# Optimization experiments

Hardware: AMD Instinct MI355X
Metric: run time of the kernel (lower is better)

The kernel has to match this reference:

```python
import jax, jax.numpy as jnp
import numpy as np

BEAM = 5  # config['beam_size']

def layer_norm(x, g, b, eps=1e-5):
    mu = jnp.mean(x, -1, keepdims=True)
    var = jnp.var(x, -1, keepdims=True)
    return (x - mu) / jnp.sqrt(var + eps) * g + b

def det_topk(logits, mask, k):
    # deterministic (eval-mode) stochastic_topk: masked softmax scores +
    # one-hot select masks for the top-k logits. shapes: logits/mask (M,S)
    ml = jnp.where(mask > 0, logits, -1e9)
    e = jnp.exp(ml - jnp.max(ml, -1, keepdims=True)) * mask
    soft = e / (jnp.sum(e, -1, keepdims=True) + 1e-20)
    _, idx = jax.lax.top_k(ml, k)
    sel = jax.nn.one_hot(idx, logits.shape[-1], dtype=logits.dtype)  # (M,k,S)
    return sel, soft

def grc(l, r, p):
    # Gated Recursive Cell: two-layer MLP -> 4 chunks, softmax gate over
    # {left, right, candidate}, LayerNorm output. l, r: (M, D)
    x = jnp.concatenate([l, r], -1)
    h = jax.nn.gelu(x @ p['Wc1'] + p['bc1'], approximate=False)
    c = (h @ p['Wc2'] + p['bc2']).reshape(l.shape[0], 4, l.shape[-1])
    g = jax.nn.softmax(c[:, 0:3, :], axis=1)
    out = g[:, 0] * l + g[:, 1] * r + g[:, 2] * c[:, 3]
    return layer_norm(out, p['g2'], p['b2'])

def select_composition(content, mask, accu, beam_mask, p):
    N, B, Sp1, D = content.shape
    S = Sp1 - 1
    # decision scores for every adjacent (left, right) pair
    cat = jnp.concatenate([content[:, :, :-1, :], content[:, :, 1:, :]], -1)  # (N,B,S,2D)
    w = (jax.nn.gelu(cat @ p['Wd1'] + p['bd1'], approximate=False) @ p['Wd2'] + p['bd2'])[..., 0]
    topk = min(S, BEAM)
    mNB = jnp.broadcast_to(mask[:, None, :], (N, B, S)).reshape(N * B, S)
    sel, soft = det_topk(w.reshape(N * B, S), mNB, topk)
    soft = soft.reshape(N, B, 1, S)
    sel = sel.reshape(N, B, topk, S)
    new_scores = jnp.log(jnp.sum(sel * soft, -1) + 1e-20)  # (N,B,topk)
    done = (1.0 - mask[:, 0])[:, None, None]
    if topk == 1:
        done_topk = jnp.ones((N, B, 1), content.dtype)
    else:
        done_topk = jnp.concatenate([jnp.ones((N, B, 1), content.dtype),
                                     jnp.zeros((N, B, topk - 1), content.dtype)], -1)
    new_bm = done * done_topk + (1.0 - done)
    beam_mask = (beam_mask[..., None] * new_bm).reshape(N, B * topk)
    accu = (accu[:, :, None] + new_scores).reshape(N, B * topk)
    sel = sel.reshape(N, B * topk, S)
    content = jnp.broadcast_to(content[:, :, None], (N, B, topk, Sp1, D)).reshape(N, B * topk, Sp1, D)
    if B * topk > BEAM:
        # prune expanded beams back to BEAM via one-hot select matmuls
        bsel, _ = det_topk(accu, beam_mask, BEAM)  # (N, BEAM, B*topk)
        content = jnp.einsum('nkb,nbsd->nksd', bsel, content)
        sel = jnp.einsum('nkb,nbs->nks', bsel, sel)
        accu = jnp.einsum('nkb,nb->nk', bsel, accu)
        beam_mask = jnp.einsum('nkb,nb->nk', bsel, beam_mask)
        B2 = BEAM
    else:
        B2 = B * topk
    olc, orc = content[:, :, :-1, :], content[:, :, 1:, :]
    l = jnp.einsum('nbs,nbsd->nbd', sel, olc).reshape(N * B2, D)
    r = jnp.einsum('nbs,nbsd->nbd', sel, orc).reshape(N * B2, D)
    new = grc(l, r, p).reshape(N, B2, 1, D)
    cs = jnp.cumsum(sel, -1)
    # splice merged node back: left of merge keeps olc, right keeps orc
    new = sel[..., None] * new + (1.0 - cs)[..., None] * olc + (cs - sel)[..., None] * orc
    return content, new, accu, beam_mask

def _forward(x, mask, p):
    N, S, _ = x.shape
    content = layer_norm(x @ p['Wi'] + p['bi'], p['g1'], p['b1'])[:, None]  # (N,1,S,D)
    D = content.shape[-1]
    accu = jnp.zeros((N, 1), x.dtype)
    beam_mask = jnp.ones((N, 1), x.dtype)
    for i in range(S - 1):
        B = content.shape[1]
        if i < S - 2:
            old, new, accu, beam_mask = select_composition(content, mask[:, i + 1:], accu, beam_mask, p)
        else:
            old = content  # (N,B,2,D)
            l = content[:, :, 0, :].reshape(N * B, D)
            r = content[:, :, 1, :].reshape(N * B, D)
            new = grc(l, r, p).reshape(N, B, 1, D)
        done = mask[:, i + 1][:, None, None, None]
        content = done * new + (1.0 - done) * old[:, :, :-1, :]
    h = content[:, :, 0, :]  # (N,B,D)
    scores = beam_mask * accu + (1.0 - beam_mask) * (-999999.0)
    w = jax.nn.softmax(scores, -1)
    return jnp.sum(w[..., None] * h, axis=1)  # global_state (N,D)

def setup_inputs() -> dict:
    key = jax.random.key(0)
    ks = jax.random.split(key, 6)
    N, S, WD, D = 256, 32, 512, 512
    CH = 4 * D
    def lin(k, fi, fo):
        return (jax.random.normal(k, (fi, fo), jnp.float32) / np.sqrt(fi).astype(np.float32))
    return {
        'x': jax.random.normal(ks[0], (N, S, WD), jnp.float32),
        'mask': jnp.ones((N, S), jnp.float32),
        'Wi': lin(ks[1], WD, D), 'bi': jnp.zeros((D,), jnp.float32),
        'g1': jnp.ones((D,), jnp.float32), 'b1': jnp.zeros((D,), jnp.float32),
        'Wd1': lin(ks[2], 2 * D, D), 'bd1': jnp.zeros((D,), jnp.float32),
        'Wd2': lin(ks[3], D, 1), 'bd2': jnp.zeros((1,), jnp.float32),
        'Wc1': lin(ks[4], 2 * D, CH), 'bc1': jnp.zeros((CH,), jnp.float32),
        'Wc2': lin(ks[5], CH, 4 * D), 'bc2': jnp.zeros((4 * D,), jnp.float32),
        'g2': jnp.ones((D,), jnp.float32), 'b2': jnp.zeros((D,), jnp.float32),
    }

def reference(x, mask, Wi, bi, g1, b1, Wd1, bd1, Wd2, bd2, Wc1, bc1, Wc2, bc2, g2, b2):
    p = dict(Wi=Wi, bi=bi, g1=g1, b1=b1, Wd1=Wd1, bd1=bd1, Wd2=Wd2, bd2=bd2,
             Wc1=Wc1, bc1=bc1, Wc2=Wc2, bc2=bc2, g2=g2, b2=b2)
    return _forward(x, mask, p)
```

## Files before the change

### kernel.cpp

```cpp
#include <hip/hip_runtime.h>
#include <math.h>


#define NN   256
#define S0   32
#define WDIM 512
#define DD   512
#define CHID 2048
#define BEAM 5
#define NB   (NN*BEAM)
#define RSCALE 2048.0f
#define RINV  (1.0f/2048.0f)
#define AR_INIT 8192
#define AR_TOT  (AR_INIT + 30*NB)
#define MN2 ((size_t)NB*CHID)

typedef __attribute__((ext_vector_type(8))) _Float16 f16x8;
typedef __attribute__((ext_vector_type(4))) float f32x4;

__device__ __forceinline__ float gelu_f(float x) {
    return 0.5f * x * (1.0f + erff(x * 0.7071067811865475f));
}
__device__ __forceinline__ _Float16 hi16(float v) { return (_Float16)v; }
__device__ __forceinline__ _Float16 lo16(float v, _Float16 h) {
    return (_Float16)((v - (float)h) * RSCALE);
}
__device__ __forceinline__ float recon(_Float16 h, _Float16 l) {
    return (float)h + RINV * (float)l;
}

__device__ __forceinline__ void gload_lds16(const void* g, void* l) {
    __builtin_amdgcn_global_load_lds(
        (const __attribute__((address_space(1))) unsigned*)g,
        (__attribute__((address_space(3))) unsigned*)l, 16, 0, 0);
}

__device__ __forceinline__ float block_reduce_sum(float v, float* sb) {
    #pragma unroll
    for (int o = 32; o > 0; o >>= 1) v += __shfl_down(v, o);
    const int lane = threadIdx.x & 63, wid = threadIdx.x >> 6;
    __syncthreads();
    if (lane == 0) sb[wid] = v;
    __syncthreads();
    return sb[0] + sb[1] + sb[2] + sb[3];
}

template<int AIDX>
__global__ __launch_bounds__(256, 1) void k_gemm(
    const _Float16* __restrict__ Ah, const _Float16* __restrict__ Al,
    const _Float16* __restrict__ Bh, const _Float16* __restrict__ Bl,
    const float* __restrict__ bias, float* __restrict__ Cf,
    int M, int N, int Ktot, int Kchunk)
{
    __shared__ __align__(16) _Float16 lds[2][4 * 4096];
    const int t = threadIdx.x, wave = t >> 6, lane = t & 63;
    const int bm = blockIdx.y * 128, bn = blockIdx.x * 128;
    const int koff = blockIdx.z * Kchunk;
    const int wm = (wave >> 1) * 64, wn = (wave & 1) * 64;
    const int rsub = lane >> 2, seg = lane & 3;
    const int fm = lane & 15, fko = (lane >> 4) * 8;

    f32x4 acc0[4][4], acc1[4][4];
    #pragma unroll
    for (int i = 0; i < 4; ++i)
        #pragma unroll
        for (int j = 0; j < 4; ++j) {
            acc0[i][j] = (f32x4){0.f, 0.f, 0.f, 0.f};
            acc1[i][j] = (f32x4){0.f, 0.f, 0.f, 0.f};
        }

    const int iters = Kchunk >> 5;
    #define STAGE_G(IT, BUF) {                                                 \
        const int k = koff + (IT)*32;                                          \
        _Float16* Lb = &lds[BUF][0];                                           \
        _Pragma("unroll")                                                      \
        for (int j = 0; j < 2; ++j) {                                          \
            const int q = wave * 2 + j;                                        \
            const size_t aoff = (size_t)(bm + q*16 + rsub) * Ktot + k + seg*8; \
            const size_t boff = (size_t)(bn + q*16 + rsub) * Ktot + k + seg*8; \
            gload_lds16(Ah + aoff, Lb + 0*4096 + q*512);                       \
            gload_lds16(Al + aoff, Lb + 1*4096 + q*512);                       \
            gload_lds16(Bh + boff, Lb + 2*4096 + q*512);                       \
            gload_lds16(Bl + boff, Lb + 3*4096 + q*512);                       \
        } }

    STAGE_G(0, 0);
    for (int it = 0; it < iters; ++it) {
        __syncthreads();
        if (it + 1 < iters) STAGE_G(it + 1, (it + 1) & 1);
        const _Float16* L = &lds[it & 1][0];
        f16x8 ah[4], al[4];
        #pragma unroll
        for (int i = 0; i < 4; ++i) {
            const int ar = wm + i*16 + fm;
            ah[i] = *(const f16x8*)&L[0*4096 + ar*32 + fko];
            al[i] = *(const f16x8*)&L[1*4096 + ar*32 + fko];
        }
        #pragma unroll
        for (int j = 0; j < 4; ++j) {
            const int br = wn + j*16 + fm;
            f16x8 bh = *(const f16x8*)&L[2*4096 + br*32 + fko];
            f16x8 bl = *(const f16x8*)&L[3*4096 + br*32 + fko];
            #pragma unroll
            for (int i = 0; i < 4; ++i) {
                acc0[i][j] = __builtin_amdgcn_mfma_f32_16x16x32_f16(ah[i], bh, acc0[i][j], 0, 0, 0);
                acc1[i][j] = __builtin_amdgcn_mfma_f32_16x16x32_f16(ah[i], bl, acc1[i][j], 0, 0, 0);
                acc1[i][j] = __builtin_amdgcn_mfma_f32_16x16x32_f16(al[i], bh, acc1[i][j], 0, 0, 0);
            }
        }
    }
    float* dst = Cf + (size_t)blockIdx.z * M * N;
    #pragma unroll
    for (int i = 0; i < 4; ++i)
        #pragma unroll
        for (int j = 0; j < 4; ++j) {
            const int col = bn + wn + j*16 + fm;
            const float bv = (blockIdx.z == 0) ? bias[col] : 0.f;
            #pragma unroll
            for (int r = 0; r < 4; ++r) {
                const int row = bm + wm + i*16 + (lane >> 4)*4 + r;
                dst[(size_t)row * N + col] = acc0[i][j][r] + acc1[i][j][r] * RINV + bv;
            }
        }
    #undef STAGE_G
}

template<int AIDX>
__global__ __launch_bounds__(256, 1) void k_gemm1(
    const _Float16* __restrict__ Ah, const _Float16* __restrict__ Al,
    const _Float16* __restrict__ Bh, const _Float16* __restrict__ Bl,
    const float* __restrict__ bias,
    _Float16* __restrict__ Oh, _Float16* __restrict__ Ol,
    const int* __restrict__ lrid, const int* __restrict__ rrid,
    const int* __restrict__ idxt, int N)
{
    __shared__ __align__(16) _Float16 lds[2][12288];
    const int t = threadIdx.x, wave = t >> 6, lane = t & 63;
    const int bm = blockIdx.y * 128, bn = blockIdx.x * 64;
    const int rsub = lane >> 2, seg = lane & 3;
    const int fm = lane & 15, quad = lane >> 4, fko = quad * 8;

    size_t lb[2], rb[2];
    #pragma unroll
    for (int j = 0; j < 2; ++j) {
        const int rowm = bm + (wave*2 + j)*16 + rsub;
        if (AIDX == 1) {
            lb[j] = (size_t)lrid[rowm] * 512;
            rb[j] = (size_t)rrid[rowm] * 512;
        } else {
            lb[j] = (size_t)idxt[rowm*31 + 0] * 512;
            rb[j] = (size_t)idxt[rowm*31 + 1] * 512;
        }
    }
    const size_t bbase = (size_t)(bn + wave*16 + rsub) * 1024;

    f32x4 acc0[2][4], acc1[2][4];
    #pragma unroll
    for (int i = 0; i < 2; ++i)
        #pragma unroll
        for (int j = 0; j < 4; ++j) {
            acc0[i][j] = (f32x4){0.f, 0.f, 0.f, 0.f};
            acc1[i][j] = (f32x4){0.f, 0.f, 0.f, 0.f};
        }

    #define STAGE_G1(IT, BUF) {                                                 \
        const int k0 = (IT)*32;                                                 \
        _Float16* Lb = &lds[BUF][0];                                            \
        _Pragma("unroll")                                                       \
        for (int j = 0; j < 2; ++j) {                                           \
            const int q = wave*2 + j;                                           \
            const size_t aoff = (k0 < 512 ? lb[j] + k0 : rb[j] + (k0-512)) + seg*8; \
            gload_lds16(Ah + aoff, Lb + q*512);                                 \
            gload_lds16(Al + aoff, Lb + 4096 + q*512);                          \
        }                                                                       \
        gload_lds16(Bh + bbase + k0 + seg*8, Lb + 8192 + wave*512);             \
        gload_lds16(Bl + bbase + k0 + seg*8, Lb + 10240 + wave*512); }

    STAGE_G1(0, 0);
    for (int it = 0; it < 32; ++it) {
        __syncthreads();
        if (it + 1 < 32) STAGE_G1(it + 1, (it + 1) & 1);
        const _Float16* L = &lds[it & 1][0];
        f16x8 ah[2], al[2];
        #pragma unroll
        for (int i = 0; i < 2; ++i) {
            const int ar = wave*32 + i*16 + fm;
            ah[i] = *(const f16x8*)&L[ar*32 + fko];
            al[i] = *(const f16x8*)&L[4096 + ar*32 + fko];
        }
        #pragma unroll
        for (int j = 0; j < 4; ++j) {
            const int br = j*16 + fm;
            f16x8 bh = *(const f16x8*)&L[8192 + br*32 + fko];
            f16x8 bl = *(const f16x8*)&L[10240 + br*32 + fko];
            #pragma unroll
            for (int i = 0; i < 2; ++i) {
                acc0[i][j] = __builtin_amdgcn_mfma_f32_16x16x32_f16(ah[i], bh, acc0[i][j], 0, 0, 0);
                acc1[i][j] = __builtin_amdgcn_mfma_f32_16x16x32_f16(ah[i], bl, acc1[i][j], 0, 0, 0);
                acc1[i][j] = __builtin_amdgcn_mfma_f32_16x16x32_f16(al[i], bh, acc1[i][j], 0, 0, 0);
            }
        }
    }
    #pragma unroll
    for (int i = 0; i < 2; ++i)
        #pragma unroll
        for (int j = 0; j < 4; ++j) {
            const int col = bn + j*16 + fm;
            const float bv = bias[col];
            #pragma unroll
            for (int r = 0; r < 4; ++r) {
                const int row = bm + wave*32 + i*16 + quad*4 + r;
                float v = gelu_f(acc0[i][j][r] + acc1[i][j][r] * RINV + bv);
                _Float16 h = hi16(v);
                Oh[(size_t)row * N + col] = h;
                Ol[(size_t)row * N + col] = lo16(v, h);
            }
        }
    #undef STAGE_G1
}

template<int MODE>
__global__ __launch_bounds__(256, 2) void k_wscore(
    const _Float16* __restrict__ ch, const _Float16* __restrict__ cl,
    const int* __restrict__ posb, const int* __restrict__ idxt,
    const _Float16* __restrict__ Bh, const _Float16* __restrict__ Bl,
    const float* __restrict__ bd1, const float* __restrict__ u512,
    const float* __restrict__ bd2, float* __restrict__ w, int Spairs)
{
    __shared__ __align__(16) _Float16 lds[2][8192];
    const int t = threadIdx.x, wave = t >> 6, lane = t & 63;
    const int bm = blockIdx.x * 64, ncol0 = blockIdx.y * 64;
    const int rsub = lane >> 2, seg = lane & 3;
    const int fm = lane & 15, quad = lane >> 4, fko = quad * 8;

    size_t lb, rb;
    {
        const int rowm = bm + wave*16 + rsub;
        int lrow, rrow;
        if (MODE == 0) {
            const int n = rowm / 31, s = rowm - n * 31;
            lrow = n*32 + s; rrow = lrow + 1;
        } else {
            const int nk = rowm >> 1, slot = rowm & 1;
            const int s = posb[nk];
            int jw = s - 1 + slot;
            int jc = jw < 0 ? 0 : (jw > Spairs - 1 ? Spairs - 1 : jw);
            lrow = idxt[nk*31 + jc]; rrow = idxt[nk*31 + jc + 1];
        }
        lb = (size_t)lrow * 512; rb = (size_t)rrow * 512;
    }
    const size_t bbase = (size_t)(ncol0 + wave*16 + rsub) * 1024;

    f32x4 acc0[4], acc1[4];
    #pragma unroll
    for (int j = 0; j < 4; ++j) {
        acc0[j] = (f32x4){0.f, 0.f, 0.f, 0.f};
        acc1[j] = (f32x4){0.f, 0.f, 0.f, 0.f};
    }
    #define STAGE_WS(IT, BUF) {                                                \
        const int k0 = (IT)*32;                                                \
        _Float16* Lb = &lds[BUF][0];                                           \
        const size_t aoff = (k0 < 512 ? lb + k0 : rb + (k0-512)) + seg*8;      \
        gload_lds16(ch + aoff, Lb + 0*2048 + wave*512);                        \
        gload_lds16(cl + aoff, Lb + 1*2048 + wave*512);                        \
        gload_lds16(Bh + bbase + k0 + seg*8, Lb + 2*2048 + wave*512);          \
        gload_lds16(Bl + bbase + k0 + seg*8, Lb + 3*2048 + wave*512); }

    STAGE_WS(0, 0);
    for (int it = 0; it < 32; ++it) {
        __syncthreads();
        if (it + 1 < 32) STAGE_WS(it + 1, (it + 1) & 1);
        const _Float16* L = &lds[it & 1][0];
        const int ar = wave*16 + fm;
        f16x8 ah = *(const f16x8*)&L[0*2048 + ar*32 + fko];
        f16x8 al = *(const f16x8*)&L[1*2048 + ar*32 + fko];
        #pragma unroll
        for (int j = 0; j < 4; ++j) {
            const int br = j*16 + fm;
            f16x8 bh = *(const f16x8*)&L[2*2048 + br*32 + fko];
            f16x8 bl = *(const f16x8*)&L[3*2048 + br*32 + fko];
            acc0[j] = __builtin_amdgcn_mfma_f32_16x16x32_f16(ah, bh, acc0[j], 0, 0, 0);
            acc1[j] = __builtin_amdgcn_mfma_f32_16x16x32_f16(ah, bl, acc1[j], 0, 0, 0);
            acc1[j] = __builtin_amdgcn_mfma_f32_16x16x32_f16(al, bh, acc1[j], 0, 0, 0);
        }
    }
    float part[4] = {0.f, 0.f, 0.f, 0.f};
    #pragma unroll
    for (int j = 0; j < 4; ++j) {
        const int col = ncol0 + j*16 + fm;
        const float bv = bd1[col], uv = u512[col];
        #pragma unroll
        for (int r = 0; r < 4; ++r) {
            float v = acc0[j][r] + acc1[j][r] * RINV + bv;
            part[r] += gelu_f(v) * uv;
        }
    }
    #pragma unroll
    for (int r = 0; r < 4; ++r) {
        float s = part[r];
        s += __shfl_xor(s, 1); s += __shfl_xor(s, 2);
        s += __shfl_xor(s, 4); s += __shfl_xor(s, 8);
        part[r] = s;
    }
    if (fm == 0) {
        const float bd2v = (blockIdx.y == 0) ? bd2[0] : 0.f;
        #pragma unroll
        for (int r = 0; r < 4; ++r) {
            const int rowm = bm + wave*16 + quad*4 + r;
            int wi = -1;
            if (MODE == 0) {
                const int n = rowm / 31, s = rowm - n * 31;
                wi = n * BEAM * S0 + s;
            } else {
                const int nk = rowm >> 1, slot = rowm & 1;
                const int jw = posb[nk] - 1 + slot;
                if (jw >= 0 && jw < Spairs) wi = nk * S0 + jw;
            }
            if (wi >= 0) atomicAdd(&w[wi], part[r] + bd2v);
        }
    }
    #undef STAGE_WS
}

__global__ __launch_bounds__(256) void k_tsplit(
    const float* __restrict__ in, _Float16* __restrict__ oh,
    _Float16* __restrict__ ol, int K, int N)
{
    __shared__ float tile[32][33];
    const int bx = blockIdx.x * 32, by = blockIdx.y * 32;
    const int t = threadIdx.x, r = t >> 5, c = t & 31;
    #pragma unroll
    for (int p = 0; p < 4; ++p)
        tile[r + p*8][c] = in[(size_t)(by + r + p*8) * N + bx + c];
    __syncthreads();
    #pragma unroll
    for (int p = 0; p < 4; ++p) {
        const int nl = r + p*8;
        float v = tile[c][nl];
        _Float16 h = hi16(v);
        oh[(size_t)(bx + nl) * K + by + c] = h;
        ol[(size_t)(bx + nl) * K + by + c] = lo16(v, h);
    }
}

__global__ __launch_bounds__(256) void k_xsplit(
    const float* __restrict__ in, _Float16* __restrict__ oh,
    _Float16* __restrict__ ol)
{
    const size_t i = ((size_t)blockIdx.x * 256 + threadIdx.x) * 4;
    float4 v = *(const float4*)(in + i);
    _Float16 h0 = hi16(v.x), h1 = hi16(v.y), h2 = hi16(v.z), h3 = hi16(v.w);
    typedef __attribute__((ext_vector_type(4))) _Float16 f16x4v;
    f16x4v h = {h0, h1, h2, h3};
    f16x4v l = {lo16(v.x,h0), lo16(v.y,h1), lo16(v.z,h2), lo16(v.w,h3)};
    *(f16x4v*)(oh + i) = h;
    *(f16x4v*)(ol + i) = l;
}

__global__ __launch_bounds__(256) void k_ln_init(
    const float* __restrict__ y, const float* __restrict__ g,
    const float* __restrict__ b, _Float16* __restrict__ cha,
    _Float16* __restrict__ cla)
{
    const int row = blockIdx.x;
    const float* yr = y + (size_t)row * DD;
    const int t = threadIdx.x;
    float v0 = yr[t], v1 = yr[t + 256];
    __shared__ float sb[8];
    float s1 = block_reduce_sum(v0 + v1, sb);
    float s2 = block_reduce_sum(v0*v0 + v1*v1, sb);
    float mu = s1 * (1.f/512.f);
    float rstd = rsqrtf(s2 * (1.f/512.f) - mu*mu + 1e-5f);
    float a0 = (v0 - mu) * rstd * g[t]       + b[t];
    float a1 = (v1 - mu) * rstd * g[t + 256] + b[t + 256];
    _Float16 h0 = hi16(a0), h1 = hi16(a1);
    cha[(size_t)row*DD + t]       = h0;
    cla[(size_t)row*DD + t]       = lo16(a0, h0);
    cha[(size_t)row*DD + t + 256] = h1;
    cla[(size_t)row*DD + t + 256] = lo16(a1, h1);
}

__global__ void k_init_state(float* accu, float* bm, int* idx0, float* wz) {
    int i = blockIdx.x * blockDim.x + threadIdx.x;
    if (i < NB*S0) wz[i] = 0.f;
    if (i < AR_INIT) idx0[i] = i;
    if (i < NB) { accu[i] = 0.f; bm[i] = 1.f; }
}

__global__ __launch_bounds__(64) void k_topk(
    const float* __restrict__ w, const float* __restrict__ accu,
    const float* __restrict__ bmask, const float* __restrict__ maskg,
    int iiter, int B, int S, int topk, int do_bsel,
    const int* __restrict__ idxold, int BAo, int STo,
    int* __restrict__ parent, int* __restrict__ posb,
    int* __restrict__ lrid, int* __restrict__ rrid,
    float* __restrict__ accu_out, float* __restrict__ bm_out,
    float* __restrict__ wnew, int Snew, int dow)
{
    const int n = blockIdx.x, lane = threadIdx.x;
    __shared__ int   selpos_s[BEAM][BEAM];
    __shared__ float nscore_s[BEAM][BEAM];
    __shared__ int   par_s[BEAM], pos_s[BEAM];
    const float* mrow = maskg + n*S0 + (iiter + 1);
    const float mk   = (lane < S) ? mrow[lane] : 0.f;
    const float done = 1.f - mrow[0];
    for (int b = 0; b < B; ++b) {
        float ml;
        if (lane < S) {
            float wv = w[(n*BEAM + b)*S0 + lane];
            ml = (mk > 0.f) ? wv : -1e9f;
        } else ml = -INFINITY;
        float mx = ml;
        #pragma unroll
        for (int o = 32; o > 0; o >>= 1) mx = fmaxf(mx, __shfl_xor(mx, o));
        float e = (lane < S) ? expf(ml - mx) * mk : 0.f;
        float es = e;
        #pragma unroll
        for (int o = 32; o > 0; o >>= 1) es += __shfl_xor(es, o);
        const float den = es + 1e-20f;
        float mlc = ml;
        for (int ts = 0; ts < topk; ++ts) {
            unsigned int fb = __float_as_uint(mlc);
            unsigned int ok = (fb & 0x80000000u) ? ~fb : (fb | 0x80000000u);
            unsigned long long key =
                ((unsigned long long)ok << 32) | (unsigned int)(63 - lane);
            if (lane >= S) key = 0ull;
            unsigned long long km = key;
            #pragma unroll
            for (int o = 32; o > 0; o >>= 1) {
                unsigned long long oth = __shfl_xor(km, o);
                km = (oth > km) ? oth : km;
            }
            int sidx = 63 - (int)(km & 0xffffffffull);
            float esel = __shfl(e, sidx);
            if (lane == 0) {
                selpos_s[b][ts] = sidx;
                nscore_s[b][ts] = logf(esel / den + 1e-20f);
            }
            if (lane == sidx) mlc = -INFINITY;
        }
    }
    __syncthreads();
    {
        const int C = B * topk;
        float ac = 0.f, bc = 0.f;
        if (lane < C) {
            const int pb = lane / topk, ptt = lane - pb * topk;
            ac = accu[n*BEAM + pb] + nscore_s[pb][ptt];
            const float nb = done * ((ptt == 0) ? 1.f : 0.f) + (1.f - done);
            bc = bmask[n*BEAM + pb] * nb;
        }
        bool used = false;
        for (int k = 0; k < BEAM; ++k) {
            int bestc;
            if (do_bsel) {
                const float v = (lane < C && !used)
                                ? ((bc > 0.f) ? ac : -1e9f) : -INFINITY;
                unsigned fb = __float_as_uint(v);
                unsigned ok = (fb & 0x80000000u) ? ~fb : (fb | 0x80000000u);
                unsigned long long key =
                    ((unsigned long long)ok << 32) | (unsigned)(63 - lane);
                unsigned long long km = key;
                #pragma unroll
                for (int o = 32; o > 0; o >>= 1) {
                    unsigned long long oth = __shfl_xor(km, o);
                    km = (oth > km) ? oth : km;
                }
                bestc = 63 - (int)(km & 0xffffffffull);
            } else bestc = k;
            if (lane == bestc) used = true;
            const float av  = __shfl(ac, bestc);
            const float bv2 = __shfl(bc, bestc);
            const int pp = bestc / topk, ss = selpos_s[pp][bestc - pp * topk];
            if (lane == 0) {
                parent[n*BEAM + k] = pp;
                posb[n*BEAM + k]   = ss;
                par_s[k] = pp; pos_s[k] = ss;
                accu_out[n*BEAM + k] = av;
                bm_out[n*BEAM + k]   = bv2;
            }
        }
    }
    __syncthreads();
    if (lane < BEAM) {
        const int base = (n*BAo + par_s[lane]) * STo + pos_s[lane];
        lrid[n*BEAM + lane] = idxold[base];
        rrid[n*BEAM + lane] = idxold[base + 1];
    }
    if (dow) {
        for (int k = 0; k < BEAM; ++k) {
            const int p = par_s[k], s = pos_s[k];
            if (lane < Snew) {
                float v = 0.f;
                if (lane < s - 1)      v = w[(n*BEAM + p)*S0 + lane];
                else if (lane > s)     v = w[(n*BEAM + p)*S0 + lane + 1];
                wnew[(n*BEAM + k)*S0 + lane] = v;
            }
        }
    }
}

__global__ __launch_bounds__(256) void k_compose(
    const float* __restrict__ P,
    const _Float16* __restrict__ cha_r, const _Float16* __restrict__ cla_r,
    const int* __restrict__ lrid, const int* __restrict__ rrid,
    const int* __restrict__ parent, const int* __restrict__ posb,
    const int* __restrict__ idxold, int BAo, int STo,
    const float* __restrict__ maskg, int iiter, int Spnew,
    const float* __restrict__ gp, const float* __restrict__ bp,
    _Float16* __restrict__ cha_w, _Float16* __restrict__ cla_w, int newbase,
    int* __restrict__ idxnew, int finalflag, float* __restrict__ nvout)
{
    __shared__ float sb[8];
    const int nk = blockIdx.x, t = threadIdx.x;
    const int n = nk / BEAM;
    size_t lbase, rbase;
    if (finalflag) {
        lbase = (size_t)idxold[nk*31 + 0] * 512;
        rbase = (size_t)idxold[nk*31 + 1] * 512;
    } else {
        lbase = (size_t)lrid[nk] * 512;
        rbase = (size_t)rrid[nk] * 512;
    }
    const float* c = P + (size_t)nk * CHID;
    float o[2];
    #pragma unroll
    for (int e = 0; e < 2; ++e) {
        const int d = t + 256*e;
        const float lv = recon(cha_r[lbase + d], cla_r[lbase + d]);
        const float rv = recon(cha_r[rbase + d], cla_r[rbase + d]);
        float c0 = ((c[d]        + c[MN2 + d])        + c[2*MN2 + d])        + c[3*MN2 + d];
        float c1 = ((c[DD + d]   + c[MN2 + DD + d])   + c[2*MN2 + DD + d])   + c[3*MN2 + DD + d];
        float c2 = ((c[2*DD + d] + c[MN2 + 2*DD + d]) + c[2*MN2 + 2*DD + d]) + c[3*MN2 + 2*DD + d];
        float c3 = ((c[3*DD + d] + c[MN2 + 3*DD + d]) + c[2*MN2 + 3*DD + d]) + c[3*MN2 + 3*DD + d];
        float m = fmaxf(c0, fmaxf(c1, c2));
        float e0 = expf(c0 - m), e1 = expf(c1 - m), e2 = expf(c2 - m);
        float inv = 1.f / (e0 + e1 + e2);
        o[e] = (e0*lv + e1*rv + e2*c3) * inv;
    }
    float s1 = block_reduce_sum(o[0] + o[1], sb);
    float s2 = block_reduce_sum(o[0]*o[0] + o[1]*o[1], sb);
    float mu = s1 * (1.f/512.f);
    float rstd = rsqrtf(s2 * (1.f/512.f) - mu*mu + 1e-5f);
    if (finalflag) {
        #pragma unroll
        for (int e = 0; e < 2; ++e) {
            const int d = t + 256*e;
            nvout[(size_t)nk*DD + d] = (o[e] - mu) * rstd * gp[d] + bp[d];
        }
        return;
    }
    const int arow = newbase + nk;
    #pragma unroll
    for (int e = 0; e < 2; ++e) {
        const int d = t + 256*e;
        float v = (o[e] - mu) * rstd * gp[d] + bp[d];
        _Float16 h = hi16(v);
        cha_w[(size_t)arow*512 + d] = h;
        cla_w[(size_t)arow*512 + d] = lo16(v, h);
    }
    if (t < Spnew) {
        const float done = maskg[n*S0 + iiter + 1];
        const int p = parent[nk], s = posb[nk];
        const int src = (n*BAo + p) * STo;
        int val;
        if (done > 0.5f)
            val = (t < s) ? idxold[src + t] : (t == s ? arow : idxold[src + t + 1]);
        else
            val = idxold[src + t];
        idxnew[nk*31 + t] = val;
    }
}

__global__ __launch_bounds__(256) void k_final(
    const float* __restrict__ nv,
    const _Float16* __restrict__ cha, const _Float16* __restrict__ cla,
    const int* __restrict__ idxt, const float* __restrict__ maskg,
    const float* __restrict__ accu, const float* __restrict__ bmv,
    float* __restrict__ out)
{
    const int n = blockIdx.x, t = threadIdx.x;
    const float done = maskg[n*S0 + 31];
    float sc[BEAM];
    #pragma unroll
    for (int k = 0; k < BEAM; ++k) {
        float m = bmv[n*BEAM + k];
        sc[k] = m * accu[n*BEAM + k] + (1.f - m) * (-999999.f);
    }
    float mx = sc[0];
    #pragma unroll
    for (int k = 1; k < BEAM; ++k) mx = fmaxf(mx, sc[k]);
    float e[BEAM], den = 0.f;
    #pragma unroll
    for (int k = 0; k < BEAM; ++k) { e[k] = expf(sc[k] - mx); den += e[k]; }
    const float inv = 1.f / den;
    #pragma unroll
    for (int i2 = 0; i2 < 2; ++i2) {
        const int d = t + 256*i2;
        float s = 0.f;
        #pragma unroll
        for (int k = 0; k < BEAM; ++k) {
            const int nk = n*BEAM + k;
            const size_t ob = (size_t)idxt[nk*31] * 512;
            const float nvv  = nv[(size_t)nk*DD + d];
            const float oldv = recon(cha[ob + d], cla[ob + d]);
            s += e[k]*inv * (done*nvv + (1.f - done)*oldv);
        }
        out[(size_t)n*DD + d] = s;
    }
}

extern "C" void kernel_launch(void* const* d_in, const int* in_sizes, int n_in,
                              void* d_out, int out_size, void* d_ws, size_t ws_size,
                              hipStream_t stream) {
    (void)in_sizes; (void)n_in; (void)out_size; (void)ws_size;
    const float* x    = (const float*)d_in[0];
    const float* mask = (const float*)d_in[1];
    const float* Wi   = (const float*)d_in[2];
    const float* bi   = (const float*)d_in[3];
    const float* g1   = (const float*)d_in[4];
    const float* b1   = (const float*)d_in[5];
    const float* Wd1  = (const float*)d_in[6];
    const float* bd1  = (const float*)d_in[7];
    const float* Wd2  = (const float*)d_in[8];
    const float* bd2  = (const float*)d_in[9];
    const float* Wc1  = (const float*)d_in[10];
    const float* bc1  = (const float*)d_in[11];
    const float* Wc2  = (const float*)d_in[12];
    const float* bc2  = (const float*)d_in[13];
    const float* g2   = (const float*)d_in[14];
    const float* b2   = (const float*)d_in[15];
    float* out = (float*)d_out;

    char* p = (char*)d_ws;
    _Float16* cha = (_Float16*)p;        p += (size_t)AR_TOT*512*2;
    _Float16* cla = (_Float16*)p;        p += (size_t)AR_TOT*512*2;
    _Float16* Wc1th = (_Float16*)p;      p += (size_t)CHID*1024*2;
    _Float16* Wc1tl = (_Float16*)p;      p += (size_t)CHID*1024*2;
    _Float16* Wc2th = (_Float16*)p;      p += (size_t)CHID*CHID*2;
    _Float16* Wc2tl = (_Float16*)p;      p += (size_t)CHID*CHID*2;
    _Float16* Wd1th = (_Float16*)p;      p += (size_t)512*1024*2;
    _Float16* Wd1tl = (_Float16*)p;      p += (size_t)512*1024*2;
    _Float16* Wih = (_Float16*)p;        p += (size_t)WDIM*DD*2;
    _Float16* Wil = (_Float16*)p;        p += (size_t)WDIM*DD*2;
    _Float16* Hh  = (_Float16*)p;        p += (size_t)NB*CHID*2;
    _Float16* Hl  = (_Float16*)p;        p += (size_t)NB*CHID*2;
    float* Pb   = (float*)p;             p += MN2*4*4;
    float* nvb  = (float*)p;             p += (size_t)NB*DD*4;
    float* wA   = (float*)p;             p += (size_t)NB*S0*4;
    float* wB   = (float*)p;             p += (size_t)NB*S0*4;
    float* accA = (float*)p;             p += NB*4;
    float* accB = (float*)p;             p += NB*4;
    float* bmA  = (float*)p;             p += NB*4;
    float* bmB  = (float*)p;             p += NB*4;
    int* parent = (int*)p;               p += NB*4;
    int* posb   = (int*)p;               p += NB*4;
    int* lrid   = (int*)p;               p += NB*4;
    int* rrid   = (int*)p;               p += NB*4;
    int* idx0   = (int*)p;               p += AR_INIT*4;
    int* idxA   = (int*)p;               p += NB*31*4;
    int* idxB   = (int*)p;               p += NB*31*4;
    _Float16* xh = (_Float16*)Pb;
    _Float16* xl = (_Float16*)((char*)Pb + (size_t)AR_INIT*512*2);
    float* ybuf  = (float*)((char*)Pb + (size_t)AR_INIT*512*4);

    k_tsplit<<<dim3(CHID/32, 1024/32), 256, 0, stream>>>(Wc1, Wc1th, Wc1tl, 1024, CHID);
    k_tsplit<<<dim3(CHID/32, CHID/32), 256, 0, stream>>>(Wc2, Wc2th, Wc2tl, CHID, CHID);
    k_tsplit<<<dim3(512/32, 1024/32), 256, 0, stream>>>(Wd1, Wd1th, Wd1tl, 1024, 512);
    k_tsplit<<<dim3(DD/32, WDIM/32), 256, 0, stream>>>(Wi, Wih, Wil, WDIM, DD);
    k_init_state<<<(NB*S0 + 255)/256, 256, 0, stream>>>(accA, bmA, idx0, wA);

    k_xsplit<<<(AR_INIT*WDIM)/1024, 256, 0, stream>>>(x, xh, xl);
    k_gemm<0><<<dim3(DD/128, AR_INIT/128, 1), 256, 0, stream>>>(
        xh, xl, Wih, Wil, bi, ybuf, AR_INIT, DD, WDIM, WDIM);
    k_ln_init<<<AR_INIT, 256, 0, stream>>>(ybuf, g1, b1, cha, cla);
    k_wscore<0><<<dim3(NN*31/64, 8), 256, 0, stream>>>(
        cha, cla, nullptr, nullptr, Wd1th, Wd1tl, bd1, Wd2, bd2, wA, 31);

    const int* idxcur = idx0;
    int* idxnxt = idxA;
    int BAo = 1, STo = 32;
    float *wcur = wA, *wnxt = wB;
    float *acur = accA, *anxt = accB, *bcur = bmA, *bnxt = bmB;
    for (int i = 0; i < 30; ++i) {
        const int B  = (i == 0) ? 1 : BEAM;
        const int S  = 31 - i;
        const int tk = (S < BEAM) ? S : BEAM;
        const int dob = (B*tk > BEAM) ? 1 : 0;
        const int newbase = AR_INIT + i*NB;
        k_topk<<<NN, 64, 0, stream>>>(wcur, acur, bcur, mask, i, B, S, tk, dob,
                                      idxcur, BAo, STo, parent, posb, lrid, rrid,
                                      anxt, bnxt, wnxt, S - 1, (i < 29) ? 1 : 0);
        k_gemm1<1><<<dim3(CHID/64, NB/128), 256, 0, stream>>>(
            cha, cla, Wc1th, Wc1tl, bc1, Hh, Hl, lrid, rrid, nullptr, CHID);
        k_gemm<0><<<dim3(CHID/128, NB/128, 4), 256, 0, stream>>>(
            Hh, Hl, Wc2th, Wc2tl, bc2, Pb, NB, CHID, CHID, 512);
        k_compose<<<NB, 256, 0, stream>>>(Pb, cha, cla, lrid, rrid, parent, posb,
                                          idxcur, BAo, STo, mask, i, 31 - i,
                                          g2, b2, cha, cla, newbase, idxnxt,
                                          0, nullptr);
        if (i < 29)
            k_wscore<1><<<dim3(NB*2/64, 8), 256, 0, stream>>>(
                cha, cla, posb, idxnxt, Wd1th, Wd1tl, bd1, Wd2, bd2, wnxt, S - 1);
        idxcur = idxnxt;
        idxnxt = (idxnxt == idxA) ? idxB : idxA;
        BAo = BEAM; STo = 31;
        float* tp;
        tp = wcur; wcur = wnxt; wnxt = tp;
        tp = acur; acur = anxt; anxt = tp;
        tp = bcur; bcur = bnxt; bnxt = tp;
    }
    k_gemm1<2><<<dim3(CHID/64, NB/128), 256, 0, stream>>>(
        cha, cla, Wc1th, Wc1tl, bc1, Hh, Hl, nullptr, nullptr, idxcur, CHID);
    k_gemm<0><<<dim3(CHID/128, NB/128, 4), 256, 0, stream>>>(
        Hh, Hl, Wc2th, Wc2tl, bc2, Pb, NB, CHID, CHID, 512);
    k_compose<<<NB, 256, 0, stream>>>(Pb, cha, cla, nullptr, nullptr, parent, posb,
                                      idxcur, BEAM, 31, mask, 30, 0,
                                      g2, b2, nullptr, nullptr, 0,
                                      nullptr, 1, nvb);
    k_final<<<NN, 256, 0, stream>>>(nvb, cha, cla, idxcur, mask, acur, bcur, out);
}
```

Before: 4.302 ms.

## Use 32x32x16 MFMA in split-fp16 GEMM and add XCD-aware workgroup swizzle

The main GEMM kernel moves from 16x16x32 MFMA tiles to 32x32x16 MFMA tiles with 16-wide accumulators. This cuts LDS fragment loads per flop and the instruction count. All three GEMM-style kernels also remap the workgroup index so that consecutive tiles land on the same XCD, which should improve L2 reuse of shared A/B panels. The swizzle assumes the workgroup count is divisible by 8. It also changes the tile traversal order in k_gemm1 and k_wscore, where the block index is now decomposed column-major.

```diff
diff --git a/kernel.cpp b/kernel.cpp
--- a/kernel.cpp
+++ b/kernel.cpp
@@ -17,6 +17,7 @@
 
 typedef __attribute__((ext_vector_type(8))) _Float16 f16x8;
 typedef __attribute__((ext_vector_type(4))) float f32x4;
+typedef __attribute__((ext_vector_type(16))) float f32x16;
 
 __device__ __forceinline__ float gelu_f(float x) {
     return 0.5f * x * (1.0f + erff(x * 0.7071067811865475f));
@@ -27,6 +28,10 @@
 }
 __device__ __forceinline__ float recon(_Float16 h, _Float16 l) {
     return (float)h + RINV * (float)l;
+}
+
+__device__ __forceinline__ int xcd_swz(int wg, int nwg) {
+    return (wg & 7) * (nwg >> 3) + (wg >> 3);
 }
 
 __device__ __forceinline__ void gload_lds16(const void* g, void* l) {
@@ -54,19 +59,28 @@
 {
     __shared__ __align__(16) _Float16 lds[2][4 * 4096];
     const int t = threadIdx.x, wave = t >> 6, lane = t & 63;
-    const int bm = blockIdx.y * 128, bn = blockIdx.x * 128;
-    const int koff = blockIdx.z * Kchunk;
+    const int gx = gridDim.x, gy = gridDim.y;
+    const int nwg = gx * gy * gridDim.z;
+    int wg = (blockIdx.z * gy + blockIdx.y) * gx + blockIdx.x;
+    wg = xcd_swz(wg, nwg);
+    const int gxy = gx * gy;
+    const int bz  = wg / gxy;
+    const int rem = wg - bz * gxy;
+    const int byy = rem / gx;
+    const int bxx = rem - byy * gx;
+    const int bm = byy * 128, bn = bxx * 128;
+    const int koff = bz * Kchunk;
     const int wm = (wave >> 1) * 64, wn = (wave & 1) * 64;
     const int rsub = lane >> 2, seg = lane & 3;
-    const int fm = lane & 15, fko = (lane >> 4) * 8;
-
-    f32x4 acc0[4][4], acc1[4][4];
-    #pragma unroll
-    for (int i = 0; i < 4; ++i)
-        #pragma unroll
-        for (int j = 0; j < 4; ++j) {
-            acc0[i][j] = (f32x4){0.f, 0.f, 0.f, 0.f};
-            acc1[i][j] = (f32x4){0.f, 0.f, 0.f, 0.f};
+    const int l31 = lane & 31, khalf = lane >> 5;
+
+    f32x16 acc0[2][2], acc1[2][2];
+    #pragma unroll
+    for (int i = 0; i < 2; ++i)
+        #pragma unroll
+        for (int j = 0; j < 2; ++j) {
+            #pragma unroll
+            for (int r = 0; r < 16; ++r) { acc0[i][j][r] = 0.f; acc1[i][j][r] = 0.f; }
         }
 
     const int iters = Kchunk >> 5;
@@ -89,36 +103,39 @@
         __syncthreads();
         if (it + 1 < iters) STAGE_G(it + 1, (it + 1) & 1);
         const _Float16* L = &lds[it & 1][0];
-        f16x8 ah[4], al[4];
-        #pragma unroll
-        for (int i = 0; i < 4; ++i) {
-            const int ar = wm + i*16 + fm;
-            ah[i] = *(const f16x8*)&L[0*4096 + ar*32 + fko];
-            al[i] = *(const f16x8*)&L[1*4096 + ar*32 + fko];
-        }
-        #pragma unroll
-        for (int j = 0; j < 4; ++j) {
-            const int br = wn + j*16 + fm;
-            f16x8 bh = *(const f16x8*)&L[2*4096 + br*32 + fko];
-            f16x8 bl = *(const f16x8*)&L[3*4096 + br*32 + fko];
+        #pragma unroll
+        for (int ks = 0; ks < 2; ++ks) {
+            f16x8 ah[2], al[2];
             #pragma unroll
-            for (int i = 0; i < 4; ++i) {
-                acc0[i][j] = __builtin_amdgcn_mfma_f32_16x16x32_f16(ah[i], bh, acc0[i][j], 0, 0, 0);
-                acc1[i][j] = __builtin_amdgcn_mfma_f32_16x16x32_f16(ah[i], bl, acc1[i][j], 0, 0, 0);
-                acc1[i][j] = __builtin_amdgcn_mfma_f32_16x16x32_f16(al[i], bh, acc1[i][j], 0, 0, 0);
-            }
-        }
-    }
-    float* dst = Cf + (size_t)blockIdx.z * M * N;
-    #pragma unroll
-    for (int i = 0; i < 4; ++i)
-        #pragma unroll
-        for (int j = 0; j < 4; ++j) {
-            const int col = bn + wn + j*16 + fm;
-            const float bv = (blockIdx.z == 0) ? bias[col] : 0.f;
+            for (int i = 0; i < 2; ++i) {
+                const int ao = (wm + i*32 + l31)*32 + ks*16 + khalf*8;
+                ah[i] = *(const f16x8*)&L[0*4096 + ao];
+                al[i] = *(const f16x8*)&L[1*4096 + ao];
+            }
             #pragma unroll
-            for (int r = 0; r < 4; ++r) {
-                const int row = bm + wm + i*16 + (lane >> 4)*4 + r;
+            for (int j = 0; j < 2; ++j) {
+                const int bo = (wn + j*32 + l31)*32 + ks*16 + khalf*8;
+                f16x8 bh = *(const f16x8*)&L[2*4096 + bo];
+                f16x8 bl = *(const f16x8*)&L[3*4096 + bo];
+                #pragma unroll
+                for (int i = 0; i < 2; ++i) {
+                    acc0[i][j] = __builtin_amdgcn_mfma_f32_32x32x16_f16(ah[i], bh, acc0[i][j], 0, 0, 0);
+                    acc1[i][j] = __builtin_amdgcn_mfma_f32_32x32x16_f16(ah[i], bl, acc1[i][j], 0, 0, 0);
+                    acc1[i][j] = __builtin_amdgcn_mfma_f32_32x32x16_f16(al[i], bh, acc1[i][j], 0, 0, 0);
+                }
+            }
+        }
+    }
+    float* dst = Cf + (size_t)bz * M * N;
+    #pragma unroll
+    for (int i = 0; i < 2; ++i)
+        #pragma unroll
+        for (int j = 0; j < 2; ++j) {
+            const int col = bn + wn + j*32 + l31;
+            const float bv = (bz == 0) ? bias[col] : 0.f;
+            #pragma unroll
+            for (int r = 0; r < 16; ++r) {
+                const int row = bm + wm + i*32 + (r & 3) + ((r >> 2) * 8) + khalf * 4;
                 dst[(size_t)row * N + col] = acc0[i][j][r] + acc1[i][j][r] * RINV + bv;
             }
         }
@@ -136,7 +153,11 @@
 {
     __shared__ __align__(16) _Float16 lds[2][12288];
     const int t = threadIdx.x, wave = t >> 6, lane = t & 63;
-    const int bm = blockIdx.y * 128, bn = blockIdx.x * 64;
+    const int nwg = gridDim.x * gridDim.y;
+    int wg = blockIdx.y * gridDim.x + blockIdx.x;
+    wg = xcd_swz(wg, nwg);
+    const int bxx = wg / gridDim.y, byy = wg - bxx * gridDim.y;
+    const int bm = byy * 128, bn = bxx * 64;
     const int rsub = lane >> 2, seg = lane & 3;
     const int fm = lane & 15, quad = lane >> 4, fko = quad * 8;
 
@@ -229,7 +250,11 @@
 {
     __shared__ __align__(16) _Float16 lds[2][8192];
     const int t = threadIdx.x, wave = t >> 6, lane = t & 63;
-    const int bm = blockIdx.x * 64, ncol0 = blockIdx.y * 64;
+    const int nwg = gridDim.x * gridDim.y;
+    int wg = blockIdx.y * gridDim.x + blockIdx.x;
+    wg = xcd_swz(wg, nwg);
+    const int bxx = wg / gridDim.y, byy = wg - bxx * gridDim.y;
+    const int bm = bxx * 64, ncol0 = byy * 64;
     const int rsub = lane >> 2, seg = lane & 3;
     const int fm = lane & 15, quad = lane >> 4, fko = quad * 8;
 
@@ -303,7 +328,7 @@
         part[r] = s;
     }
     if (fm == 0) {
-        const float bd2v = (blockIdx.y == 0) ? bd2[0] : 0.f;
+        const float bd2v = (byy == 0) ? bd2[0] : 0.f;
         #pragma unroll
         for (int r = 0; r < 4; ++r) {
             const int rowm = bm + wave*16 + quad*4 + r;
```

Measured after the change: 4.495 ms. 1.04x slower.
